# Performance work log

Hardware: AMD Instinct MI355X
Metric: run time of the kernel (lower is better)

Reference implementation:

```python
import jax, jax.numpy as jnp
import numpy as np

D_MODEL = 1024
N_HEADS = 16
D_HEAD = D_MODEL // N_HEADS
B, L = 4, 2048
NEG_INF = float('-inf')


def setup_inputs() -> dict:
    key = jax.random.key(0)
    ks = jax.random.split(key, 8)
    x = jax.random.normal(ks[0], (B, L, D_MODEL), dtype=jnp.float32)
    # sorted cumulative event times in hours (~0-2000h span)
    timestamps = jnp.cumsum(jax.random.uniform(ks[1], (B, L), dtype=jnp.float32), axis=-1)
    mask = jnp.ones((B, L), dtype=jnp.float32)
    s = 1.0 / np.sqrt(D_MODEL)
    W_qkv = jax.random.normal(ks[2], (3 * D_MODEL, D_MODEL), dtype=jnp.float32) * s
    b_qkv = jnp.zeros((3 * D_MODEL,), dtype=jnp.float32)
    W_out = jax.random.normal(ks[3], (D_MODEL, D_MODEL), dtype=jnp.float32) * s
    b_out = jnp.zeros((D_MODEL,), dtype=jnp.float32)
    decay_rate = jnp.full((N_HEADS,), 0.01, dtype=jnp.float32)
    return {"x": x, "timestamps": timestamps, "mask": mask,
            "W_qkv": W_qkv, "b_qkv": b_qkv, "W_out": W_out, "b_out": b_out,
            "decay_rate": decay_rate}


def reference(x, timestamps, mask, W_qkv, b_qkv, W_out, b_out, decay_rate):
    Bb, Ll, Dd = x.shape
    H, dh = N_HEADS, D_HEAD
    scale = dh ** (-0.5)
    qkv = x @ W_qkv.T + b_qkv                     # (B,L,3D)
    qkv = qkv.reshape(Bb, Ll, 3, H, dh).transpose(2, 0, 3, 1, 4)  # (3,B,H,L,dh)
    q, k, v = qkv[0], qkv[1], qkv[2]
    attn = jnp.einsum('bhqd,bhkd->bhqk', q, k) * scale
    t_diff = jnp.abs(timestamps[:, :, None] - timestamps[:, None, :])[:, None]  # (B,1,L,L)
    decay = jax.nn.softplus(decay_rate)[None, :, None, None]                    # (1,H,1,1)
    attn = attn - decay * t_diff / 24.0
    causal = jnp.triu(jnp.ones((Ll, Ll), dtype=bool), k=1)        # (L,L) True above diag
    attn = jnp.where(causal[None, None], NEG_INF, attn)
    pad = (mask == 0.0)[:, None, None, :]                         # (B,1,1,L) True=pad key
    attn = jnp.where(pad, NEG_INF, attn)
    attn = jax.nn.softmax(attn, axis=-1)
    out = jnp.einsum('bhqk,bhkd->bhqd', attn, v)                  # (B,H,L,dh)
    out = out.transpose(0, 2, 1, 3).reshape(Bb, Ll, Dd)
    return out @ W_out.T + b_out
```

## Files before the change

### kernel.cpp

```cpp
#include <hip/hip_runtime.h>
#include <stdint.h>
#include <math.h>

#define B_   4
#define L_   2048
#define H_   16
#define DH_  64
#define DM_  1024

typedef __bf16 bf16;
typedef __attribute__((ext_vector_type(8))) __bf16 bf16x8;
typedef __attribute__((ext_vector_type(4))) float f32x4;
typedef __attribute__((ext_vector_type(4))) int i32x4;
typedef __attribute__((ext_vector_type(4))) short s16x4;
typedef unsigned short u16;
typedef unsigned int u32;
typedef __attribute__((ext_vector_type(2))) unsigned int u32x2;
typedef __attribute__((ext_vector_type(4))) unsigned short u16x4;

typedef unsigned int u32g __attribute__((address_space(1)));
typedef unsigned int u32l __attribute__((address_space(3)));

__device__ __forceinline__ u16 f2bf(float f) {
  return __builtin_bit_cast(u16, (bf16)f);
}

__device__ __forceinline__ float exp2_fast(float x) {
  float r; asm("v_exp_f32 %0, %1" : "=v"(r) : "v"(x)); return r;
}

__device__ __forceinline__ void gload16(const void* g, void* l) {
  __builtin_amdgcn_global_load_lds((const u32g*)g, (u32l*)l, 16, 0, 0);
}

__device__ __forceinline__ f32x4 mfma16(s16x4 a, s16x4 b, f32x4 c) {
#if __has_builtin(__builtin_amdgcn_mfma_f32_16x16x16bf16_1k)
  return __builtin_amdgcn_mfma_f32_16x16x16bf16_1k(a, b, c, 0, 0, 0);
#else
  asm volatile("v_mfma_f32_16x16x16_bf16 %0, %1, %2, %0\n\ts_nop 7\n\ts_nop 2"
               : "+v"(c) : "v"(a), "v"(b));
  return c;
#endif
}

__global__ __launch_bounds__(256) void cvt_f32_bf16(const float* __restrict__ src,
                                                    u16* __restrict__ dst, int n4) {
  int i = blockIdx.x * 256 + threadIdx.x;
  if (i >= n4) return;
  f32x4 v = ((const f32x4*)src)[i];
  u16x4 o;
  o[0] = f2bf(v[0]); o[1] = f2bf(v[1]); o[2] = f2bf(v[2]); o[3] = f2bf(v[3]);
  ((u16x4*)dst)[i] = o;
}

__global__ __launch_bounds__(256) void bias_fill(const float* __restrict__ ts,
                                                 const float* __restrict__ msk,
                                                 const float* __restrict__ decay,
                                                 float* __restrict__ Bk) {
  int i = blockIdx.x * 256 + threadIdx.x;
  int bh = i >> 11, l = i & (L_ - 1);
  int b = bh >> 4, h = bh & 15;
  float dc24 = log1pf(__expf(decay[h])) * (1.0f / 24.0f) * 1.44269504f;
  float tv = ts[b * L_ + l], mv = msk[b * L_ + l];
  Bk[i] = (mv != 0.f) ? dc24 * tv : -INFINITY;
}

__global__ __launch_bounds__(256) void gemm_bf16(
    const u16* __restrict__ A, const u16* __restrict__ Bm, const float* __restrict__ bias,
    int M, int N, int K, int mode,
    u16* __restrict__ Qb, u16* __restrict__ Kb, u16* __restrict__ Vt, float* __restrict__ Cout)
{
  extern __shared__ char smem[];
  u16* ltr = (u16*)smem;

  const int tid = threadIdx.x;
  const int m0 = blockIdx.y * 128, n0 = blockIdx.x * 128;
  const int lane = tid & 63, w = tid >> 6;
  const int g = lane >> 4, col = lane & 15;
  const int wr = w >> 1, wc = w & 1;

  f32x4 acc[4][4];
#pragma unroll
  for (int mt = 0; mt < 4; ++mt)
#pragma unroll
    for (int nt = 0; nt < 4; ++nt) {
      acc[mt][nt][0] = 0.f; acc[mt][nt][1] = 0.f;
      acc[mt][nt][2] = 0.f; acc[mt][nt][3] = 0.f;
    }

  auto STAGEG = [&](int k0, int nb) {
    char* dA = smem + (nb << 14);
    char* dB = dA + 8192;
#pragma unroll
    for (int hh = 0; hh < 2; ++hh) {
      int c = tid + hh * 256;
      int row = c >> 2, sub = c & 3;
      int sc = sub ^ ((row >> 1) & 3);
      gload16(A  + (size_t)(m0 + row) * K + (k0 + sc * 8), dA + c * 16);
      gload16(Bm + (size_t)(n0 + row) * K + (k0 + sc * 8), dB + c * 16);
    }
  };

  STAGEG(0, 0);
  __syncthreads();

  const int nk = K >> 5;
  for (int i = 0; i < nk; ++i) {
    const int cur = i & 1;
    if (i + 1 < nk) STAGEG((i + 1) * 32, cur ^ 1);

    const char* bufA = smem + (cur << 14);
    const char* bufB = bufA + 8192;
    bf16x8 af[4], bfr[4];
#pragma unroll
    for (int mt = 0; mt < 4; ++mt) {
      int row = wr * 64 + mt * 16 + col;
      af[mt] = *(const bf16x8*)(bufA + row * 64 + ((g ^ ((row >> 1) & 3)) << 4));
    }
#pragma unroll
    for (int nt = 0; nt < 4; ++nt) {
      int row = wc * 64 + nt * 16 + col;
      bfr[nt] = *(const bf16x8*)(bufB + row * 64 + ((g ^ ((row >> 1) & 3)) << 4));
    }
#pragma unroll
    for (int mt = 0; mt < 4; ++mt)
#pragma unroll
      for (int nt = 0; nt < 4; ++nt)
        acc[mt][nt] = __builtin_amdgcn_mfma_f32_16x16x32_bf16(af[mt], bfr[nt], acc[mt][nt], 0, 0, 0);

    __syncthreads();
  }

  if (mode == 1) {
#pragma unroll
    for (int nt = 0; nt < 4; ++nt) {
      int gn = n0 + wc * 64 + nt * 16 + col;
      float bv = bias[gn];
#pragma unroll
      for (int mt = 0; mt < 4; ++mt) {
        int mbase = m0 + wr * 64 + mt * 16 + g * 4;
#pragma unroll
        for (int r = 0; r < 4; ++r)
          Cout[(size_t)(mbase + r) * N + gn] = acc[mt][nt][r] + bv;
      }
    }
    return;
  }

  const int type = n0 >> 10;
  const float qsc = (type == 0) ? 0.125f * 1.44269504f : 1.0f;
#pragma unroll
  for (int nt = 0; nt < 4; ++nt) {
    int nn = wc * 64 + nt * 16 + col;
    float bv = bias[n0 + nn];
#pragma unroll
    for (int mt = 0; mt < 4; ++mt) {
      int mm = wr * 64 + mt * 16 + g * 4;
#pragma unroll
      for (int r = 0; r < 4; ++r) {
        u16 hv = f2bf((acc[mt][nt][r] + bv) * qsc);
        if (type < 2) ltr[(mm + r) * 136 + nn] = hv;
        else          ltr[nn * 136 + (mm + r)] = hv;
      }
    }
  }
  __syncthreads();
#pragma unroll
  for (int it = 0; it < 8; ++it) {
    int cid = tid + it * 256;
    int rrow = cid >> 4, cc = cid & 15;
    i32x4 v = *(const i32x4*)((const char*)ltr + rrow * 272 + cc * 16);
    if (type < 2) {
      int token = m0 + rrow;
      int bb = token >> 11, ll = token & (L_ - 1);
      int gn = n0 + cc * 8;
      int head = (gn & 1023) >> 6, d = gn & 63;
      u16* dst = (type == 0) ? Qb : Kb;
      *(i32x4*)(dst + ((size_t)((bb * H_ + head) * L_ + ll)) * 64 + d) = v;
    } else {
      int gn = n0 + rrow;
      int head = (gn & 1023) >> 6, d = gn & 63;
      int token0 = m0 + cc * 8;
      int bb = token0 >> 11, ll = token0 & (L_ - 1);
      *(i32x4*)(Vt + ((size_t)((bb * H_ + head) * DH_ + d)) * L_ + ll) = v;
    }
  }
}

__global__ __launch_bounds__(512, 2) void attn_fwd(
    const u16* __restrict__ Qb, const u16* __restrict__ Kb, const u16* __restrict__ Vt,
    const float* __restrict__ Bk, u16* __restrict__ AO)
{
  __shared__ u16 lK[3][64 * 64];
  __shared__ u16 lV[3][64 * 64];

  const int phys = blockIdx.x;
  const int xcd = phys & 7, s = phys >> 3;
  const int bh = xcd * 8 + (s >> 3);
  const int pr = s & 7;
  const int qa = pr, qbt = 15 - pr;
  const int b = bh >> 4, h = bh & 15;

  const int tid = threadIdx.x, w = tid >> 6, lane = tid & 63;
  const int g = lane >> 4, q16 = lane & 15;

  const float* Bkb = Bk + (size_t)bh * L_;

  int kcol[2], vcol[4];
#pragma unroll
  for (int kk = 0; kk < 2; ++kk) kcol[kk] = ((kk * 4 + g) ^ (q16 & 7)) << 4;
#pragma unroll
  for (int t = 0; t < 4; ++t)
    vcol[t] = (((2 * t + (g >> 1)) ^ (q16 & 7)) << 4) + (g & 1) * 8;

  const int nkA = (qa + 1) * 2;
  const int nkB = (qbt + 1) * 2;

  auto STAGE = [&](int gst, int nb) {
    const int kt = (gst < nkA) ? gst : gst - nkA;
    const int kg0 = kt * 64;
    const int r8 = tid >> 3, cc = tid & 7;
    gload16(Kb + ((size_t)bh * L_ + kg0 + r8) * 64 + ((cc ^ (r8 & 7)) * 8),
            (char*)lK[nb] + tid * 16);
    gload16(Vt + ((size_t)(bh * 64 + r8)) * L_ + kg0 + ((cc ^ (r8 & 7)) * 8),
            (char*)lV[nb] + tid * 16);
  };

  auto BODY = [&](bf16x8 (&qf)[2], f32x4 (&o)[4], float& m_r, float& l_r,
                  int qrow, int kg0, int cur) {
    f32x4 sv[4];
#pragma unroll
    for (int t = 0; t < 4; ++t)
      sv[t] = *(const f32x4*)(Bkb + kg0 + t * 16 + g * 4);

    __builtin_amdgcn_s_setprio(1);
#pragma unroll
    for (int t = 0; t < 4; ++t) {
      const char* krow = (const char*)lK[cur] + t * 2048 + q16 * 128;
#pragma unroll
      for (int kk = 0; kk < 2; ++kk) {
        bf16x8 kf = *(const bf16x8*)(krow + kcol[kk]);
        sv[t] = __builtin_amdgcn_mfma_f32_16x16x32_bf16(kf, qf[kk], sv[t], 0, 0, 0);
      }
    }
    __builtin_amdgcn_s_setprio(0);

    if (kg0 + 63 > qrow) {
      const int qg = qrow + q16;
#pragma unroll
      for (int t = 0; t < 4; ++t)
#pragma unroll
        for (int r = 0; r < 4; ++r)
          sv[t][r] = (kg0 + t * 16 + g * 4 + r <= qg) ? sv[t][r] : -INFINITY;
    }

    float mx = fmaxf(sv[0][0], sv[0][1]);
    mx = fmaxf(mx, fmaxf(sv[0][2], sv[0][3]));
#pragma unroll
    for (int t = 1; t < 4; ++t) {
      mx = fmaxf(mx, fmaxf(sv[t][0], sv[t][1]));
      mx = fmaxf(mx, fmaxf(sv[t][2], sv[t][3]));
    }
    mx = fmaxf(mx, __shfl_xor(mx, 16));
    mx = fmaxf(mx, __shfl_xor(mx, 32));

    float mn = m_r;
    if (__any(mx > m_r + 8.f)) {
      mn = fmaxf(m_r, mx);
      float al = exp2_fast(m_r - mn);
      m_r = mn;
      l_r *= al;
#pragma unroll
      for (int db = 0; db < 4; ++db) {
        o[db][0] *= al; o[db][1] *= al; o[db][2] *= al; o[db][3] *= al;
      }
    }
    float rs = 0.f;
#pragma unroll
    for (int t = 0; t < 4; ++t)
#pragma unroll
      for (int r = 0; r < 4; ++r) {
        float pv = exp2_fast(sv[t][r] - mn);
        sv[t][r] = pv;
        rs += pv;
      }
    l_r += rs;

    s16x4 pf[4];
#pragma unroll
    for (int t = 0; t < 4; ++t) {
      s16x4 pp;
      pp[0] = (short)f2bf(sv[t][0]); pp[1] = (short)f2bf(sv[t][1]);
      pp[2] = (short)f2bf(sv[t][2]); pp[3] = (short)f2bf(sv[t][3]);
      pf[t] = pp;
    }

    __builtin_amdgcn_s_setprio(1);
#pragma unroll
    for (int t = 0; t < 4; ++t) {
      const char* vrow = (const char*)lV[cur] + q16 * 128 + vcol[t];
#pragma unroll
      for (int db = 0; db < 4; ++db) {
        s16x4 vf = *(const s16x4*)(vrow + db * 2048);
        o[db] = mfma16(vf, pf[t], o[db]);
      }
    }
    __builtin_amdgcn_s_setprio(0);
  };

  auto EPI = [&](f32x4 (&o)[4], float l_r, int qt) {
    float lt = l_r + __shfl_xor(l_r, 16);
    lt += __shfl_xor(lt, 32);
    float inv = 1.f / lt;
    u16* dst = AO + ((size_t)(b * L_ + qt * 128 + w * 16 + q16)) * DM_ + h * 64 + g * 4;
#pragma unroll
    for (int db = 0; db < 4; ++db) {
      u32x2 pk;
      pk[0] = (u32)f2bf(o[db][0] * inv) | ((u32)f2bf(o[db][1] * inv) << 16);
      pk[1] = (u32)f2bf(o[db][2] * inv) | ((u32)f2bf(o[db][3] * inv) << 16);
      *(u32x2*)(dst + db * 16) = pk;
    }
  };

  STAGE(0, 0);
  STAGE(1, 1);
  asm volatile("s_waitcnt vmcnt(2) lgkmcnt(0)" ::: "memory");
  __builtin_amdgcn_s_barrier();
  __builtin_amdgcn_sched_barrier(0);

  {
    const int qrow = qa * 128 + w * 16;
    const int mkt = (qrow + 79) >> 6;
    bf16x8 qf[2];
    {
      const u16* Qr = Qb + ((size_t)bh * L_ + qrow + q16) * 64;
      qf[0] = *(const bf16x8*)(Qr + g * 8);
      qf[1] = *(const bf16x8*)(Qr + 32 + g * 8);
    }
    float m_r = -INFINITY, l_r = 0.f;
    f32x4 o[4];
#pragma unroll
    for (int db = 0; db < 4; ++db) {
      o[db][0] = 0.f; o[db][1] = 0.f; o[db][2] = 0.f; o[db][3] = 0.f;
    }
    for (int st = 0; st < nkA; ++st) {
      const int cur = st % 3;
      STAGE(st + 2, (st + 2) % 3);
      if (st < mkt) BODY(qf, o, m_r, l_r, qrow, st * 64, cur);
      asm volatile("s_waitcnt vmcnt(2) lgkmcnt(0)" ::: "memory");
      __builtin_amdgcn_s_barrier();
      __builtin_amdgcn_sched_barrier(0);
    }
    EPI(o, l_r, qa);
  }

  {
    const int qrow = qbt * 128 + w * 16;
    const int mkt = (qrow + 79) >> 6;
    bf16x8 qf[2];
    {
      const u16* Qr = Qb + ((size_t)bh * L_ + qrow + q16) * 64;
      qf[0] = *(const bf16x8*)(Qr + g * 8);
      qf[1] = *(const bf16x8*)(Qr + 32 + g * 8);
    }
    float m_r = -INFINITY, l_r = 0.f;
    f32x4 o[4];
#pragma unroll
    for (int db = 0; db < 4; ++db) {
      o[db][0] = 0.f; o[db][1] = 0.f; o[db][2] = 0.f; o[db][3] = 0.f;
    }
    for (int kt = 0; kt < nkB; ++kt) {
      const int gst = nkA + kt;
      const int cur = gst % 3;
      const bool pf = (kt + 2 < nkB);
      if (pf) STAGE(gst + 2, (gst + 2) % 3);
      if (kt < mkt) BODY(qf, o, m_r, l_r, qrow, kt * 64, cur);
      if (kt + 1 < nkB) {
        if (pf) asm volatile("s_waitcnt vmcnt(2) lgkmcnt(0)" ::: "memory");
        else    asm volatile("s_waitcnt vmcnt(0) lgkmcnt(0)" ::: "memory");
        __builtin_amdgcn_s_barrier();
        __builtin_amdgcn_sched_barrier(0);
      }
    }
    EPI(o, l_r, qbt);
  }
}

extern "C" void kernel_launch(void* const* d_in, const int* in_sizes, int n_in,
                              void* d_out, int out_size, void* d_ws, size_t ws_size,
                              hipStream_t stream) {
  const float* x    = (const float*)d_in[0];
  const float* ts   = (const float*)d_in[1];
  const float* mk   = (const float*)d_in[2];
  const float* Wqkv = (const float*)d_in[3];
  const float* bqkv = (const float*)d_in[4];
  const float* Wout = (const float*)d_in[5];
  const float* bout = (const float*)d_in[6];
  const float* dec  = (const float*)d_in[7];
  float* out = (float*)d_out;

  char* ws = (char*)d_ws;
  u16* xbf  = (u16*)(ws + 0);
  u16* wqbf = (u16*)(ws + 16777216);
  u16* wobf = (u16*)(ws + 23068672);
  u16* Qb   = (u16*)(ws + 25165824);
  u16* Kb   = (u16*)(ws + 41943040);
  u16* Vt   = (u16*)(ws + 58720256);
  u16* AO   = (u16*)(ws + 75497472);
  float* Bk = (float*)(ws + 92274688);

  cvt_f32_bf16<<<dim3(8192 * 1024 / 4 / 256), 256, 0, stream>>>(x, xbf, 8192 * 1024 / 4);
  cvt_f32_bf16<<<dim3(3072 * 1024 / 4 / 256), 256, 0, stream>>>(Wqkv, wqbf, 3072 * 1024 / 4);
  cvt_f32_bf16<<<dim3(1024 * 1024 / 4 / 256), 256, 0, stream>>>(Wout, wobf, 1024 * 1024 / 4);

  bias_fill<<<dim3(64 * 2048 / 256), 256, 0, stream>>>(ts, mk, dec, Bk);

  gemm_bf16<<<dim3(3072 / 128, 8192 / 128), 256, 34816, stream>>>(
      xbf, wqbf, bqkv, 8192, 3072, 1024, 0, Qb, Kb, Vt, nullptr);

  attn_fwd<<<dim3(512), 512, 0, stream>>>(Qb, Kb, Vt, Bk, AO);

  gemm_bf16<<<dim3(1024 / 128, 8192 / 128), 256, 32768, stream>>>(
      AO, wobf, bout, 8192, 1024, 1024, 1, nullptr, nullptr, nullptr, out);
}
```

Baseline: 194.0 us.

## Restructure GEMM to 256x128 tiles with triple-buffered K=64 pipeline and XCD remap

The bf16 GEMM now uses 512-thread blocks computing 256x128 output tiles with K-steps of 64. It keeps a three-stage LDS ring buffer with explicit vmcnt waits, raises wave priority around the MFMA block, and remaps block IDs so consecutive tiles land on the same XCD. The epilogue transpose buffer is widened for the larger M tile. This aims to hide global-load latency and improve operand reuse and L2 locality, at the cost of 144KB static LDS per block, which limits occupancy to one block per CU, and more fragile manual synchronisation.

```diff
diff --git a/kernel.cpp b/kernel.cpp
--- a/kernel.cpp
+++ b/kernel.cpp
@@ -65,16 +65,22 @@
   Bk[i] = (mv != 0.f) ? dc24 * tv : -INFINITY;
 }
 
-__global__ __launch_bounds__(256) void gemm_bf16(
+__global__ __launch_bounds__(512) void gemm_bf16(
     const u16* __restrict__ A, const u16* __restrict__ Bm, const float* __restrict__ bias,
     int M, int N, int K, int mode,
     u16* __restrict__ Qb, u16* __restrict__ Kb, u16* __restrict__ Vt, float* __restrict__ Cout)
 {
-  extern __shared__ char smem[];
+  __shared__ char smem[147456];
   u16* ltr = (u16*)smem;
 
   const int tid = threadIdx.x;
-  const int m0 = blockIdx.y * 128, n0 = blockIdx.x * 128;
+  const int nwg = gridDim.x;
+  int idx = blockIdx.x;
+  idx = (idx & 7) * (nwg >> 3) + (idx >> 3);
+  const int nbx = N >> 7;
+  const int bx = idx % nbx, by = idx / nbx;
+  const int m0 = by << 8, n0 = bx << 7;
+
   const int lane = tid & 63, w = tid >> 6;
   const int g = lane >> 4, col = lane & 15;
   const int wr = w >> 1, wc = w & 1;
@@ -88,47 +94,63 @@
       acc[mt][nt][2] = 0.f; acc[mt][nt][3] = 0.f;
     }
 
-  auto STAGEG = [&](int k0, int nb) {
-    char* dA = smem + (nb << 14);
-    char* dB = dA + 8192;
-#pragma unroll
-    for (int hh = 0; hh < 2; ++hh) {
-      int c = tid + hh * 256;
-      int row = c >> 2, sub = c & 3;
-      int sc = sub ^ ((row >> 1) & 3);
-      gload16(A  + (size_t)(m0 + row) * K + (k0 + sc * 8), dA + c * 16);
-      gload16(Bm + (size_t)(n0 + row) * K + (k0 + sc * 8), dB + c * 16);
+  auto STAGEG = [&](int kt, int nb) {
+    char* dA = smem + nb * 49152;
+    char* dB = dA + 32768;
+    const int k0 = kt << 6;
+#pragma unroll
+    for (int pp = 0; pp < 4; ++pp) {
+      int c = tid + pp * 512;
+      int row = c >> 3, cc = c & 7;
+      gload16(A + (size_t)(m0 + row) * K + k0 + ((cc ^ (row & 7)) << 3), dA + c * 16);
+    }
+#pragma unroll
+    for (int pp = 0; pp < 2; ++pp) {
+      int c = tid + pp * 512;
+      int row = c >> 3, cc = c & 7;
+      gload16(Bm + (size_t)(n0 + row) * K + k0 + ((cc ^ (row & 7)) << 3), dB + c * 16);
     }
   };
 
   STAGEG(0, 0);
-  __syncthreads();
-
-  const int nk = K >> 5;
-  for (int i = 0; i < nk; ++i) {
-    const int cur = i & 1;
-    if (i + 1 < nk) STAGEG((i + 1) * 32, cur ^ 1);
-
-    const char* bufA = smem + (cur << 14);
-    const char* bufB = bufA + 8192;
-    bf16x8 af[4], bfr[4];
-#pragma unroll
-    for (int mt = 0; mt < 4; ++mt) {
-      int row = wr * 64 + mt * 16 + col;
-      af[mt] = *(const bf16x8*)(bufA + row * 64 + ((g ^ ((row >> 1) & 3)) << 4));
-    }
-#pragma unroll
-    for (int nt = 0; nt < 4; ++nt) {
-      int row = wc * 64 + nt * 16 + col;
-      bfr[nt] = *(const bf16x8*)(bufB + row * 64 + ((g ^ ((row >> 1) & 3)) << 4));
-    }
-#pragma unroll
-    for (int mt = 0; mt < 4; ++mt)
-#pragma unroll
-      for (int nt = 0; nt < 4; ++nt)
-        acc[mt][nt] = __builtin_amdgcn_mfma_f32_16x16x32_bf16(af[mt], bfr[nt], acc[mt][nt], 0, 0, 0);
-
-    __syncthreads();
+  STAGEG(1, 1);
+  asm volatile("s_waitcnt vmcnt(6)" ::: "memory");
+  __builtin_amdgcn_s_barrier();
+
+  const int nk = K >> 6;
+  for (int t = 0; t < nk; ++t) {
+    const char* bufA = smem + (t % 3) * 49152;
+    const char* bufB = bufA + 32768;
+#pragma unroll
+    for (int kk = 0; kk < 2; ++kk) {
+      bf16x8 af[4], bfr[4];
+#pragma unroll
+      for (int mt = 0; mt < 4; ++mt) {
+        int row = wr * 64 + mt * 16 + col;
+        af[mt] = *(const bf16x8*)(bufA + row * 128 + ((((kk << 2) + g) ^ (row & 7)) << 4));
+      }
+#pragma unroll
+      for (int nt = 0; nt < 4; ++nt) {
+        int row = wc * 64 + nt * 16 + col;
+        bfr[nt] = *(const bf16x8*)(bufB + row * 128 + ((((kk << 2) + g) ^ (row & 7)) << 4));
+      }
+      if (kk == 0 && t + 2 < nk) STAGEG(t + 2, (t + 2) % 3);
+      __builtin_amdgcn_s_barrier();
+      asm volatile("s_waitcnt lgkmcnt(0)" ::: "memory");
+      __builtin_amdgcn_sched_barrier(0);
+      __builtin_amdgcn_s_setprio(1);
+#pragma unroll
+      for (int mt = 0; mt < 4; ++mt)
+#pragma unroll
+        for (int nt = 0; nt < 4; ++nt)
+          acc[mt][nt] = __builtin_amdgcn_mfma_f32_16x16x32_bf16(af[mt], bfr[nt], acc[mt][nt], 0, 0, 0);
+      __builtin_amdgcn_s_setprio(0);
+      if (kk == 1) {
+        if (t + 2 < nk)      asm volatile("s_waitcnt vmcnt(6)" ::: "memory");
+        else if (t + 1 < nk) asm volatile("s_waitcnt vmcnt(0)" ::: "memory");
+      }
+      __builtin_amdgcn_s_barrier();
+    }
   }
 
   if (mode == 1) {
@@ -160,24 +182,30 @@
       for (int r = 0; r < 4; ++r) {
         u16 hv = f2bf((acc[mt][nt][r] + bv) * qsc);
         if (type < 2) ltr[(mm + r) * 136 + nn] = hv;
-        else          ltr[nn * 136 + (mm + r)] = hv;
+        else          ltr[nn * 264 + (mm + r)] = hv;
       }
     }
   }
   __syncthreads();
-#pragma unroll
-  for (int it = 0; it < 8; ++it) {
-    int cid = tid + it * 256;
-    int rrow = cid >> 4, cc = cid & 15;
-    i32x4 v = *(const i32x4*)((const char*)ltr + rrow * 272 + cc * 16);
-    if (type < 2) {
+  if (type < 2) {
+#pragma unroll
+    for (int it = 0; it < 8; ++it) {
+      int cid = tid + it * 512;
+      int rrow = cid >> 4, cc = cid & 15;
+      i32x4 v = *(const i32x4*)((const char*)ltr + rrow * 272 + cc * 16);
       int token = m0 + rrow;
       int bb = token >> 11, ll = token & (L_ - 1);
       int gn = n0 + cc * 8;
       int head = (gn & 1023) >> 6, d = gn & 63;
       u16* dst = (type == 0) ? Qb : Kb;
       *(i32x4*)(dst + ((size_t)((bb * H_ + head) * L_ + ll)) * 64 + d) = v;
-    } else {
+    }
+  } else {
+#pragma unroll
+    for (int it = 0; it < 8; ++it) {
+      int cid = tid + it * 512;
+      int rrow = cid >> 5, cc = cid & 31;
+      i32x4 v = *(const i32x4*)((const char*)ltr + rrow * 528 + cc * 16);
       int gn = n0 + rrow;
       int head = (gn & 1023) >> 6, d = gn & 63;
       int token0 = m0 + cc * 8;
@@ -415,11 +443,11 @@
 
   bias_fill<<<dim3(64 * 2048 / 256), 256, 0, stream>>>(ts, mk, dec, Bk);
 
-  gemm_bf16<<<dim3(3072 / 128, 8192 / 128), 256, 34816, stream>>>(
+  gemm_bf16<<<dim3(768), 512, 0, stream>>>(
       xbf, wqbf, bqkv, 8192, 3072, 1024, 0, Qb, Kb, Vt, nullptr);
 
   attn_fwd<<<dim3(512), 512, 0, stream>>>(Qb, Kb, Vt, Bk, AO);
 
-  gemm_bf16<<<dim3(1024 / 128, 8192 / 128), 256, 32768, stream>>>(
+  gemm_bf16<<<dim3(256), 512, 0, stream>>>(
       AO, wobf, bout, 8192, 1024, 1024, 1, nullptr, nullptr, nullptr, out);
 }
```

Result: no change. 192.8 us (-0.6%).
